# Kernel optimization log

Hardware: AMD Instinct MI355X
Metric: run time of the kernel (lower is better)

## Reference

```python
import jax, jax.numpy as jnp
import numpy as np

B, N_Q, N_K, DIM = 4, 4096, 4096, 256
INNER = 64
N_TOPK = 3
MINUS_INF = -1e9


def setup_inputs() -> dict:
    key = jax.random.key(0)
    ks = jax.random.split(key, 5)
    q = jax.random.normal(ks[0], (B, N_Q, DIM), dtype=jnp.float32)
    k = jax.random.normal(ks[1], (B, N_K, DIM), dtype=jnp.float32)
    v = jax.random.normal(ks[2], (B, N_K, DIM), dtype=jnp.float32)
    Wq = jax.random.normal(ks[3], (DIM, INNER), dtype=jnp.float32) * 0.02
    Wk = jax.random.normal(ks[4], (DIM, INNER), dtype=jnp.float32) * 0.02
    return {"q": q, "k": k, "v": v, "Wq": Wq, "Wk": Wk}


def reference(q, k, v, Wq, Wk):
    # v is accepted but unused, matching the torch module.
    scale = INNER ** (-0.5)  # dim_head == inner_dim == 64
    qh = (q @ Wq) * scale            # [B, N_Q, 64]
    kh = k @ Wk                      # [B, N_K, 64]
    # heads = 1 -> scores [B, 1, N_Q, N_K]
    scores = jnp.einsum('bqd,bkd->bqk', qh, kh)[:, None]
    # torch.kthvalue(k=N_K - 3) == 4th-largest value per row
    thresh = jax.lax.top_k(scores, N_TOPK + 1)[0][..., N_TOPK:N_TOPK + 1]
    masked = jnp.where(scores < thresh, MINUS_INF, scores)
    return jax.nn.softmax(masked, axis=-1)
```

## Files before the change

kernel.cpp:

```cpp
#include <hip/hip_runtime.h>
#include <hip/hip_bf16.h>
#include <math.h>

typedef float v4f __attribute__((ext_vector_type(4)));
typedef short bf16x8 __attribute__((ext_vector_type(8)));
typedef float f32x16 __attribute__((ext_vector_type(16)));

#define BATCH 4
#define NQ 4096
#define NK 4096
#define DIM 256
#define INNER 64
#define NEG_INF (-3.0e38f)
#define CAP 64

__global__ __launch_bounds__(256) void proj_kernel(
    const float* __restrict__ q, const float* __restrict__ k,
    const float* __restrict__ Wq, const float* __restrict__ Wk,
    float* __restrict__ qh, float* __restrict__ kh,
    ushort* __restrict__ qhb, ushort* __restrict__ khb)
{
  __shared__ float xs[32 * 260];
  const int bid = blockIdx.x;
  const bool isq = bid < 512;
  const float* X   = isq ? q : k;
  const float* W   = isq ? Wq : Wk;
  float*   out     = isq ? qh : kh;
  const float scale = isq ? 0.125f : 1.0f;
  const int row0 = (isq ? bid : bid - 512) * 32;
  const int t = threadIdx.x;

  #pragma unroll
  for (int it = 0; it < 8; ++it) {
    int idx = it * 256 + t;
    int r = idx >> 6, dq = idx & 63;
    v4f v = *reinterpret_cast<const v4f*>(X + (size_t)(row0 + r) * DIM + dq * 4);
    *reinterpret_cast<v4f*>(&xs[r * 260 + dq * 4]) = v;
  }
  __syncthreads();

  const int i0 = (t & 15) * 4;
  const int rg = t >> 4;
  float acc[2][4];
  #pragma unroll
  for (int p = 0; p < 2; ++p)
    #pragma unroll
    for (int i = 0; i < 4; ++i) acc[p][i] = 0.f;

  for (int d0 = 0; d0 < DIM; d0 += 4) {
    v4f w0 = *reinterpret_cast<const v4f*>(W + (d0 + 0) * INNER + i0);
    v4f w1 = *reinterpret_cast<const v4f*>(W + (d0 + 1) * INNER + i0);
    v4f w2 = *reinterpret_cast<const v4f*>(W + (d0 + 2) * INNER + i0);
    v4f w3 = *reinterpret_cast<const v4f*>(W + (d0 + 3) * INNER + i0);
    #pragma unroll
    for (int p = 0; p < 2; ++p) {
      v4f x = *reinterpret_cast<const v4f*>(&xs[(rg + 16 * p) * 260 + d0]);
      #pragma unroll
      for (int i = 0; i < 4; ++i) {
        float bs = x[0] * w0[i];
        bs = fmaf(x[1], w1[i], bs);
        bs = fmaf(x[2], w2[i], bs);
        bs = fmaf(x[3], w3[i], bs);
        acc[p][i] += bs;
      }
    }
  }

  const int d  = i0 >> 4;
  const int hi = (i0 >> 3) & 1;
  const int e0 = i0 & 7;
  #pragma unroll
  for (int p = 0; p < 2; ++p) {
    v4f o;
    ushort ob[4];
    #pragma unroll
    for (int i = 0; i < 4; ++i) {
      o[i] = acc[p][i] * scale;
      __hip_bfloat16 h = __float2bfloat16(o[i]);
      ob[i] = *reinterpret_cast<ushort*>(&h);
    }
    int rr = rg + 16 * p;
    size_t row = (size_t)(row0 + rr);
    *reinterpret_cast<v4f*>(out + row * INNER + i0) = o;
    if (isq) {
      *reinterpret_cast<uint2*>(qhb + row * INNER + i0) =
          *reinterpret_cast<uint2*>(ob);
    } else {
      size_t off = (size_t)(bid - 512) * 2048 + d * 512 + hi * 256 + rr * 8 + e0;
      *reinterpret_cast<uint2*>(khb + off) = *reinterpret_cast<uint2*>(ob);
    }
  }
}

__device__ __forceinline__ void insert5(float (&v)[5], int (&ix)[5], float x, int xi) {
  bool g0 = x > v[0], g1 = x > v[1], g2 = x > v[2], g3 = x > v[3];
  v[4]  = g3 ? v[3] : x;                 ix[4] = g3 ? ix[3] : xi;
  v[3]  = g3 ? (g2 ? v[2] : x) : v[3];   ix[3] = g3 ? (g2 ? ix[2] : xi) : ix[3];
  v[2]  = g2 ? (g1 ? v[1] : x) : v[2];   ix[2] = g2 ? (g1 ? ix[1] : xi) : ix[2];
  v[1]  = g1 ? (g0 ? v[0] : x) : v[1];   ix[1] = g1 ? (g0 ? ix[0] : xi) : ix[1];
  v[0]  = g0 ? x : v[0];                 ix[0] = g0 ? xi : ix[0];
}

__device__ __forceinline__ void insert8v(float (&v)[8], float x) {
  bool g0 = x > v[0], g1 = x > v[1], g2 = x > v[2], g3 = x > v[3];
  bool g4 = x > v[4], g5 = x > v[5], g6 = x > v[6];
  v[7] = g6 ? v[6] : x;
  v[6] = g6 ? (g5 ? v[5] : x) : v[6];
  v[5] = g5 ? (g4 ? v[4] : x) : v[5];
  v[4] = g4 ? (g3 ? v[3] : x) : v[4];
  v[3] = g3 ? (g2 ? v[2] : x) : v[3];
  v[2] = g2 ? (g1 ? v[1] : x) : v[2];
  v[1] = g1 ? (g0 ? v[0] : x) : v[1];
  v[0] = g0 ? x : v[0];
}

__global__ __launch_bounds__(512) void filter_kernel(
    const ushort* __restrict__ qhb, const ushort* __restrict__ khb,
    const float* __restrict__ qh, const float* __restrict__ kh,
    float* __restrict__ out)
{
  __shared__ float qhf[32][68];
  __shared__ float sm[32][16];
  __shared__ float tau[32];
  __shared__ int   cnt[32];
  __shared__ int   cand[32][CAP];
  __shared__ float exactv[32][CAP];
  __shared__ float w5[32][5];
  __shared__ int   id5[32][6];

  const int t   = threadIdx.x;
  const int bid = blockIdx.x;
  const int wg  = (bid & 7) * 64 + (bid >> 3);
  const int b   = wg >> 7;
  const int q0  = (wg & 127) * 32;
  const int qg  = t >> 6;
  const int kg  = t & 63;
  const int ln  = kg & 31;
  const int hi  = kg >> 5;

  float* obase = out + ((size_t)b * NQ + q0) * (size_t)NK;
  const v4f z = {0.f, 0.f, 0.f, 0.f};

  if (t < 256) {
    int row = t >> 3, c8 = (t & 7) * 8;
    const float* src = qh + ((size_t)b * NQ + q0 + row) * INNER + c8;
    *reinterpret_cast<v4f*>(&qhf[row][c8])     = *reinterpret_cast<const v4f*>(src);
    *reinterpret_cast<v4f*>(&qhf[row][c8 + 4]) = *reinterpret_cast<const v4f*>(src + 4);
  }
  if (t < 32) cnt[t] = 0;

  const ushort* qptr = qhb + ((size_t)b * NQ + q0 + ln) * INNER + hi * 8;
  bf16x8 qf0 = *reinterpret_cast<const bf16x8*>(qptr);
  bf16x8 qf1 = *reinterpret_cast<const bf16x8*>(qptr + 16);
  bf16x8 qf2 = *reinterpret_cast<const bf16x8*>(qptr + 32);
  bf16x8 qf3 = *reinterpret_cast<const bf16x8*>(qptr + 48);

  const ushort* ktile = khb + ((size_t)b * 128 + qg * 16) * 2048;

  float smax = NEG_INF;
  for (int t16 = 0; t16 < 16; ++t16) {
    const ushort* tb = ktile + (size_t)t16 * 2048;
    bf16x8 k0 = *reinterpret_cast<const bf16x8*>(tb +        kg * 8);
    bf16x8 k1 = *reinterpret_cast<const bf16x8*>(tb +  512 + kg * 8);
    bf16x8 k2 = *reinterpret_cast<const bf16x8*>(tb + 1024 + kg * 8);
    bf16x8 k3 = *reinterpret_cast<const bf16x8*>(tb + 1536 + kg * 8);

    *reinterpret_cast<v4f*>(obase + (size_t)(t16 * 2)     * 2048 + t * 4) = z;
    *reinterpret_cast<v4f*>(obase + (size_t)(t16 * 2 + 1) * 2048 + t * 4) = z;

    f32x16 acc = {0.f, 0.f, 0.f, 0.f, 0.f, 0.f, 0.f, 0.f,
                  0.f, 0.f, 0.f, 0.f, 0.f, 0.f, 0.f, 0.f};
    acc = __builtin_amdgcn_mfma_f32_32x32x16_bf16(k0, qf0, acc, 0, 0, 0);
    acc = __builtin_amdgcn_mfma_f32_32x32x16_bf16(k1, qf1, acc, 0, 0, 0);
    acc = __builtin_amdgcn_mfma_f32_32x32x16_bf16(k2, qf2, acc, 0, 0, 0);
    acc = __builtin_amdgcn_mfma_f32_32x32x16_bf16(k3, qf3, acc, 0, 0, 0);

    float m0 = fmaxf(fmaxf(acc[0],  acc[1]),  fmaxf(acc[2],  acc[3]));
    float m1 = fmaxf(fmaxf(acc[4],  acc[5]),  fmaxf(acc[6],  acc[7]));
    float m2 = fmaxf(fmaxf(acc[8],  acc[9]),  fmaxf(acc[10], acc[11]));
    float m3 = fmaxf(fmaxf(acc[12], acc[13]), fmaxf(acc[14], acc[15]));
    smax = fmaxf(smax, fmaxf(fmaxf(m0, m1), fmaxf(m2, m3)));
  }
  sm[ln][qg * 2 + hi] = smax;
  __syncthreads();

  if (t < 32) {
    float rv[8];
    #pragma unroll
    for (int j = 0; j < 8; ++j) rv[j] = NEG_INF;
    #pragma unroll
    for (int s = 0; s < 16; ++s) {
      float x = sm[t][s];
      if (x > rv[7]) insert8v(rv, x);
    }
    tau[t] = rv[7];
  }
  __syncthreads();

  const float tl = tau[ln];
  for (int t16 = 0; t16 < 16; ++t16) {
    const ushort* tb = ktile + (size_t)t16 * 2048;
    bf16x8 k0 = *reinterpret_cast<const bf16x8*>(tb +        kg * 8);
    bf16x8 k1 = *reinterpret_cast<const bf16x8*>(tb +  512 + kg * 8);
    bf16x8 k2 = *reinterpret_cast<const bf16x8*>(tb + 1024 + kg * 8);
    bf16x8 k3 = *reinterpret_cast<const bf16x8*>(tb + 1536 + kg * 8);

    *reinterpret_cast<v4f*>(obase + (size_t)(32 + t16 * 2)     * 2048 + t * 4) = z;
    *reinterpret_cast<v4f*>(obase + (size_t)(32 + t16 * 2 + 1) * 2048 + t * 4) = z;

    f32x16 acc = {0.f, 0.f, 0.f, 0.f, 0.f, 0.f, 0.f, 0.f,
                  0.f, 0.f, 0.f, 0.f, 0.f, 0.f, 0.f, 0.f};
    acc = __builtin_amdgcn_mfma_f32_32x32x16_bf16(k0, qf0, acc, 0, 0, 0);
    acc = __builtin_amdgcn_mfma_f32_32x32x16_bf16(k1, qf1, acc, 0, 0, 0);
    acc = __builtin_amdgcn_mfma_f32_32x32x16_bf16(k2, qf2, acc, 0, 0, 0);
    acc = __builtin_amdgcn_mfma_f32_32x32x16_bf16(k3, qf3, acc, 0, 0, 0);

    const int kb0 = qg * 512 + t16 * 32 + 4 * hi;
#define CHK(r) { float x_ = acc[r]; \
                 if (x_ >= tl) { \
                   int p_ = atomicAdd(&cnt[ln], 1); \
                   if (p_ < CAP) cand[ln][p_] = kb0 + ((r) & 3) + 8 * ((r) >> 2); } }
    CHK(0)  CHK(1)  CHK(2)  CHK(3)
    CHK(4)  CHK(5)  CHK(6)  CHK(7)
    CHK(8)  CHK(9)  CHK(10) CHK(11)
    CHK(12) CHK(13) CHK(14) CHK(15)
#undef CHK
  }
  __syncthreads();

  {
    int row = t >> 4, j0 = t & 15;
    int n = min(cnt[row], CAP);
    for (int jj = j0; jj < n; jj += 16) {
      int idx = cand[row][jj];
      const float* kcol = kh + ((size_t)b * NK + idx) * INNER;
      float acc = 0.f;
      #pragma unroll
      for (int dd = 0; dd < INNER; dd += 4) {
        v4f kv = *reinterpret_cast<const v4f*>(kcol + dd);
        v4f qv = *reinterpret_cast<const v4f*>(&qhf[row][dd]);
        float bs = qv[0] * kv[0];
        bs = fmaf(qv[1], kv[1], bs);
        bs = fmaf(qv[2], kv[2], bs);
        bs = fmaf(qv[3], kv[3], bs);
        acc += bs;
      }
      exactv[row][jj] = acc;
    }
  }
  __syncthreads();

  if (t < 32) {
    int n = min(cnt[t], CAP);
    float rv[5]; int ri[5];
    #pragma unroll
    for (int j = 0; j < 5; ++j) { rv[j] = NEG_INF; ri[j] = 0; }
    for (int j = 0; j < n; ++j) {
      float x = exactv[t][j];
      if (x > rv[4]) insert5(rv, ri, x, cand[t][j]);
    }
    bool inc4 = (rv[4] >= rv[3]);
    float e1 = expf(rv[1] - rv[0]);
    float e2 = expf(rv[2] - rv[0]);
    float e3 = expf(rv[3] - rv[0]);
    float e4 = inc4 ? expf(rv[4] - rv[0]) : 0.0f;
    float inv = 1.0f / (1.0f + e1 + e2 + e3 + e4);
    w5[t][0] = inv;      w5[t][1] = e1 * inv;  w5[t][2] = e2 * inv;
    w5[t][3] = e3 * inv; w5[t][4] = e4 * inv;
    #pragma unroll
    for (int j = 0; j < 5; ++j) id5[t][j] = ri[j];
    id5[t][5] = inc4 ? 5 : 4;
  }
  __syncthreads();

  if (t < 160) {
    int row = t / 5, j = t % 5;
    if (j < id5[row][5])
      obase[(size_t)row * NK + id5[row][j]] = w5[row][j];
  }
}

extern "C" void kernel_launch(void* const* d_in, const int* in_sizes, int n_in,
                              void* d_out, int out_size, void* d_ws, size_t ws_size,
                              hipStream_t stream) {
  const float* q  = (const float*)d_in[0];
  const float* k  = (const float*)d_in[1];
  const float* Wq = (const float*)d_in[3];
  const float* Wk = (const float*)d_in[4];

  const size_t NE = (size_t)BATCH * NQ * INNER;
  float*  qh  = (float*)d_ws;
  float*  kh  = qh + NE;
  ushort* qhb = (ushort*)(kh + NE);
  ushort* khb = qhb + NE;

  proj_kernel<<<1024, 256, 0, stream>>>(q, k, Wq, Wk, qh, kh, qhb, khb);
  filter_kernel<<<512, 512, 0, stream>>>(qhb, khb, qh, kh, (float*)d_out);
}
```

Baseline: 120.5 us.

## Specialize extra warps to zero the output with nontemporal stores

The filter kernel grows from 512 to 768 threads. The original 512 threads now only compute scores, thresholds and the top-k softmax. The extra 256 threads zero the block's 32 output rows with nontemporal vector stores, split into five phases that match the compute path's five barriers, so every zero lands before the final scatter of softmax weights. The aim is to overlap the large zero-fill write traffic with the MFMA and selection work and to keep those stores out of cache. The larger launch bound lowers the per-thread register budget, which could cause spills or reduce occupancy.

```diff
diff --git a/kernel.cpp b/kernel.cpp
--- a/kernel.cpp
+++ b/kernel.cpp
@@ -114,7 +114,7 @@
   v[0] = g0 ? x : v[0];
 }
 
-__global__ __launch_bounds__(512) void filter_kernel(
+__global__ __launch_bounds__(768) void filter_kernel(
     const ushort* __restrict__ qhb, const ushort* __restrict__ khb,
     const float* __restrict__ qh, const float* __restrict__ kh,
     float* __restrict__ out)
@@ -133,150 +133,171 @@
   const int wg  = (bid & 7) * 64 + (bid >> 3);
   const int b   = wg >> 7;
   const int q0  = (wg & 127) * 32;
-  const int qg  = t >> 6;
-  const int kg  = t & 63;
-  const int ln  = kg & 31;
-  const int hi  = kg >> 5;
 
   float* obase = out + ((size_t)b * NQ + q0) * (size_t)NK;
   const v4f z = {0.f, 0.f, 0.f, 0.f};
 
-  if (t < 256) {
-    int row = t >> 3, c8 = (t & 7) * 8;
-    const float* src = qh + ((size_t)b * NQ + q0 + row) * INNER + c8;
-    *reinterpret_cast<v4f*>(&qhf[row][c8])     = *reinterpret_cast<const v4f*>(src);
-    *reinterpret_cast<v4f*>(&qhf[row][c8 + 4]) = *reinterpret_cast<const v4f*>(src + 4);
-  }
-  if (t < 32) cnt[t] = 0;
-
-  const ushort* qptr = qhb + ((size_t)b * NQ + q0 + ln) * INNER + hi * 8;
-  bf16x8 qf0 = *reinterpret_cast<const bf16x8*>(qptr);
-  bf16x8 qf1 = *reinterpret_cast<const bf16x8*>(qptr + 16);
-  bf16x8 qf2 = *reinterpret_cast<const bf16x8*>(qptr + 32);
-  bf16x8 qf3 = *reinterpret_cast<const bf16x8*>(qptr + 48);
-
-  const ushort* ktile = khb + ((size_t)b * 128 + qg * 16) * 2048;
-
-  float smax = NEG_INF;
-  for (int t16 = 0; t16 < 16; ++t16) {
-    const ushort* tb = ktile + (size_t)t16 * 2048;
-    bf16x8 k0 = *reinterpret_cast<const bf16x8*>(tb +        kg * 8);
-    bf16x8 k1 = *reinterpret_cast<const bf16x8*>(tb +  512 + kg * 8);
-    bf16x8 k2 = *reinterpret_cast<const bf16x8*>(tb + 1024 + kg * 8);
-    bf16x8 k3 = *reinterpret_cast<const bf16x8*>(tb + 1536 + kg * 8);
-
-    *reinterpret_cast<v4f*>(obase + (size_t)(t16 * 2)     * 2048 + t * 4) = z;
-    *reinterpret_cast<v4f*>(obase + (size_t)(t16 * 2 + 1) * 2048 + t * 4) = z;
-
-    f32x16 acc = {0.f, 0.f, 0.f, 0.f, 0.f, 0.f, 0.f, 0.f,
-                  0.f, 0.f, 0.f, 0.f, 0.f, 0.f, 0.f, 0.f};
-    acc = __builtin_amdgcn_mfma_f32_32x32x16_bf16(k0, qf0, acc, 0, 0, 0);
-    acc = __builtin_amdgcn_mfma_f32_32x32x16_bf16(k1, qf1, acc, 0, 0, 0);
-    acc = __builtin_amdgcn_mfma_f32_32x32x16_bf16(k2, qf2, acc, 0, 0, 0);
-    acc = __builtin_amdgcn_mfma_f32_32x32x16_bf16(k3, qf3, acc, 0, 0, 0);
-
-    float m0 = fmaxf(fmaxf(acc[0],  acc[1]),  fmaxf(acc[2],  acc[3]));
-    float m1 = fmaxf(fmaxf(acc[4],  acc[5]),  fmaxf(acc[6],  acc[7]));
-    float m2 = fmaxf(fmaxf(acc[8],  acc[9]),  fmaxf(acc[10], acc[11]));
-    float m3 = fmaxf(fmaxf(acc[12], acc[13]), fmaxf(acc[14], acc[15]));
-    smax = fmaxf(smax, fmaxf(fmaxf(m0, m1), fmaxf(m2, m3)));
-  }
-  sm[ln][qg * 2 + hi] = smax;
-  __syncthreads();
-
-  if (t < 32) {
-    float rv[8];
-    #pragma unroll
-    for (int j = 0; j < 8; ++j) rv[j] = NEG_INF;
-    #pragma unroll
-    for (int s = 0; s < 16; ++s) {
-      float x = sm[t][s];
-      if (x > rv[7]) insert8v(rv, x);
-    }
-    tau[t] = rv[7];
-  }
-  __syncthreads();
-
-  const float tl = tau[ln];
-  for (int t16 = 0; t16 < 16; ++t16) {
-    const ushort* tb = ktile + (size_t)t16 * 2048;
-    bf16x8 k0 = *reinterpret_cast<const bf16x8*>(tb +        kg * 8);
-    bf16x8 k1 = *reinterpret_cast<const bf16x8*>(tb +  512 + kg * 8);
-    bf16x8 k2 = *reinterpret_cast<const bf16x8*>(tb + 1024 + kg * 8);
-    bf16x8 k3 = *reinterpret_cast<const bf16x8*>(tb + 1536 + kg * 8);
-
-    *reinterpret_cast<v4f*>(obase + (size_t)(32 + t16 * 2)     * 2048 + t * 4) = z;
-    *reinterpret_cast<v4f*>(obase + (size_t)(32 + t16 * 2 + 1) * 2048 + t * 4) = z;
-
-    f32x16 acc = {0.f, 0.f, 0.f, 0.f, 0.f, 0.f, 0.f, 0.f,
-                  0.f, 0.f, 0.f, 0.f, 0.f, 0.f, 0.f, 0.f};
-    acc = __builtin_amdgcn_mfma_f32_32x32x16_bf16(k0, qf0, acc, 0, 0, 0);
-    acc = __builtin_amdgcn_mfma_f32_32x32x16_bf16(k1, qf1, acc, 0, 0, 0);
-    acc = __builtin_amdgcn_mfma_f32_32x32x16_bf16(k2, qf2, acc, 0, 0, 0);
-    acc = __builtin_amdgcn_mfma_f32_32x32x16_bf16(k3, qf3, acc, 0, 0, 0);
-
-    const int kb0 = qg * 512 + t16 * 32 + 4 * hi;
+  if (t < 512) {
+    const int qg  = t >> 6;
+    const int kg  = t & 63;
+    const int ln  = kg & 31;
+    const int hi  = kg >> 5;
+
+    if (t < 256) {
+      int row = t >> 3, c8 = (t & 7) * 8;
+      const float* src = qh + ((size_t)b * NQ + q0 + row) * INNER + c8;
+      *reinterpret_cast<v4f*>(&qhf[row][c8])     = *reinterpret_cast<const v4f*>(src);
+      *reinterpret_cast<v4f*>(&qhf[row][c8 + 4]) = *reinterpret_cast<const v4f*>(src + 4);
+    }
+    if (t < 32) cnt[t] = 0;
+
+    const ushort* qptr = qhb + ((size_t)b * NQ + q0 + ln) * INNER + hi * 8;
+    bf16x8 qf0 = *reinterpret_cast<const bf16x8*>(qptr);
+    bf16x8 qf1 = *reinterpret_cast<const bf16x8*>(qptr + 16);
+    bf16x8 qf2 = *reinterpret_cast<const bf16x8*>(qptr + 32);
+    bf16x8 qf3 = *reinterpret_cast<const bf16x8*>(qptr + 48);
+
+    const ushort* ktile = khb + ((size_t)b * 128 + qg * 16) * 2048;
+
+    float smax = NEG_INF;
+    for (int t16 = 0; t16 < 16; ++t16) {
+      const ushort* tb = ktile + (size_t)t16 * 2048;
+      bf16x8 k0 = *reinterpret_cast<const bf16x8*>(tb +        kg * 8);
+      bf16x8 k1 = *reinterpret_cast<const bf16x8*>(tb +  512 + kg * 8);
+      bf16x8 k2 = *reinterpret_cast<const bf16x8*>(tb + 1024 + kg * 8);
+      bf16x8 k3 = *reinterpret_cast<const bf16x8*>(tb + 1536 + kg * 8);
+
+      f32x16 acc = {0.f, 0.f, 0.f, 0.f, 0.f, 0.f, 0.f, 0.f,
+                    0.f, 0.f, 0.f, 0.f, 0.f, 0.f, 0.f, 0.f};
+      acc = __builtin_amdgcn_mfma_f32_32x32x16_bf16(k0, qf0, acc, 0, 0, 0);
+      acc = __builtin_amdgcn_mfma_f32_32x32x16_bf16(k1, qf1, acc, 0, 0, 0);
+      acc = __builtin_amdgcn_mfma_f32_32x32x16_bf16(k2, qf2, acc, 0, 0, 0);
+      acc = __builtin_amdgcn_mfma_f32_32x32x16_bf16(k3, qf3, acc, 0, 0, 0);
+
+      float m0 = fmaxf(fmaxf(acc[0],  acc[1]),  fmaxf(acc[2],  acc[3]));
+      float m1 = fmaxf(fmaxf(acc[4],  acc[5]),  fmaxf(acc[6],  acc[7]));
+      float m2 = fmaxf(fmaxf(acc[8],  acc[9]),  fmaxf(acc[10], acc[11]));
+      float m3 = fmaxf(fmaxf(acc[12], acc[13]), fmaxf(acc[14], acc[15]));
+      smax = fmaxf(smax, fmaxf(fmaxf(m0, m1), fmaxf(m2, m3)));
+    }
+    sm[ln][qg * 2 + hi] = smax;
+    __syncthreads();
+
+    if (t < 32) {
+      float rv[8];
+      #pragma unroll
+      for (int j = 0; j < 8; ++j) rv[j] = NEG_INF;
+      #pragma unroll
+      for (int s = 0; s < 16; ++s) {
+        float x = sm[t][s];
+        if (x > rv[7]) insert8v(rv, x);
+      }
+      tau[t] = rv[7];
+    }
+    __syncthreads();
+
+    const float tl = tau[ln];
+    for (int t16 = 0; t16 < 16; ++t16) {
+      const ushort* tb = ktile + (size_t)t16 * 2048;
+      bf16x8 k0 = *reinterpret_cast<const bf16x8*>(tb +        kg * 8);
+      bf16x8 k1 = *reinterpret_cast<const bf16x8*>(tb +  512 + kg * 8);
+      bf16x8 k2 = *reinterpret_cast<const bf16x8*>(tb + 1024 + kg * 8);
+      bf16x8 k3 = *reinterpret_cast<const bf16x8*>(tb + 1536 + kg * 8);
+
+      f32x16 acc = {0.f, 0.f, 0.f, 0.f, 0.f, 0.f, 0.f, 0.f,
+                    0.f, 0.f, 0.f, 0.f, 0.f, 0.f, 0.f, 0.f};
+      acc = __builtin_amdgcn_mfma_f32_32x32x16_bf16(k0, qf0, acc, 0, 0, 0);
+      acc = __builtin_amdgcn_mfma_f32_32x32x16_bf16(k1, qf1, acc, 0, 0, 0);
+      acc = __builtin_amdgcn_mfma_f32_32x32x16_bf16(k2, qf2, acc, 0, 0, 0);
+      acc = __builtin_amdgcn_mfma_f32_32x32x16_bf16(k3, qf3, acc, 0, 0, 0);
+
+      const int kb0 = qg * 512 + t16 * 32 + 4 * hi;
 #define CHK(r) { float x_ = acc[r]; \
                  if (x_ >= tl) { \
                    int p_ = atomicAdd(&cnt[ln], 1); \
                    if (p_ < CAP) cand[ln][p_] = kb0 + ((r) & 3) + 8 * ((r) >> 2); } }
-    CHK(0)  CHK(1)  CHK(2)  CHK(3)
-    CHK(4)  CHK(5)  CHK(6)  CHK(7)
-    CHK(8)  CHK(9)  CHK(10) CHK(11)
-    CHK(12) CHK(13) CHK(14) CHK(15)
+      CHK(0)  CHK(1)  CHK(2)  CHK(3)
+      CHK(4)  CHK(5)  CHK(6)  CHK(7)
+      CHK(8)  CHK(9)  CHK(10) CHK(11)
+      CHK(12) CHK(13) CHK(14) CHK(15)
 #undef CHK
-  }
-  __syncthreads();
-
-  {
-    int row = t >> 4, j0 = t & 15;
-    int n = min(cnt[row], CAP);
-    for (int jj = j0; jj < n; jj += 16) {
-      int idx = cand[row][jj];
-      const float* kcol = kh + ((size_t)b * NK + idx) * INNER;
-      float acc = 0.f;
-      #pragma unroll
-      for (int dd = 0; dd < INNER; dd += 4) {
-        v4f kv = *reinterpret_cast<const v4f*>(kcol + dd);
-        v4f qv = *reinterpret_cast<const v4f*>(&qhf[row][dd]);
-        float bs = qv[0] * kv[0];
-        bs = fmaf(qv[1], kv[1], bs);
-        bs = fmaf(qv[2], kv[2], bs);
-        bs = fmaf(qv[3], kv[3], bs);
-        acc += bs;
+    }
+    __syncthreads();
+
+    {
+      int row = t >> 4, j0 = t & 15;
+      int n = min(cnt[row], CAP);
+      for (int jj = j0; jj < n; jj += 16) {
+        int idx = cand[row][jj];
+        const float* kcol = kh + ((size_t)b * NK + idx) * INNER;
+        float acc = 0.f;
+        #pragma unroll
+        for (int dd = 0; dd < INNER; dd += 4) {
+          v4f kv = *reinterpret_cast<const v4f*>(kcol + dd);
+          v4f qv = *reinterpret_cast<const v4f*>(&qhf[row][dd]);
+          float bs = qv[0] * kv[0];
+          bs = fmaf(qv[1], kv[1], bs);
+          bs = fmaf(qv[2], kv[2], bs);
+          bs = fmaf(qv[3], kv[3], bs);
+          acc += bs;
+        }
+        exactv[row][jj] = acc;
       }
-      exactv[row][jj] = acc;
-    }
-  }
-  __syncthreads();
-
-  if (t < 32) {
-    int n = min(cnt[t], CAP);
-    float rv[5]; int ri[5];
-    #pragma unroll
-    for (int j = 0; j < 5; ++j) { rv[j] = NEG_INF; ri[j] = 0; }
-    for (int j = 0; j < n; ++j) {
-      float x = exactv[t][j];
-      if (x > rv[4]) insert5(rv, ri, x, cand[t][j]);
-    }
-    bool inc4 = (rv[4] >= rv[3]);
-    float e1 = expf(rv[1] - rv[0]);
-    float e2 = expf(rv[2] - rv[0]);
-    float e3 = expf(rv[3] - rv[0]);
-    float e4 = inc4 ? expf(rv[4] - rv[0]) : 0.0f;
-    float inv = 1.0f / (1.0f + e1 + e2 + e3 + e4);
-    w5[t][0] = inv;      w5[t][1] = e1 * inv;  w5[t][2] = e2 * inv;
-    w5[t][3] = e3 * inv; w5[t][4] = e4 * inv;
-    #pragma unroll
-    for (int j = 0; j < 5; ++j) id5[t][j] = ri[j];
-    id5[t][5] = inc4 ? 5 : 4;
-  }
-  __syncthreads();
-
-  if (t < 160) {
-    int row = t / 5, j = t % 5;
-    if (j < id5[row][5])
-      obase[(size_t)row * NK + id5[row][j]] = w5[row][j];
+    }
+    __syncthreads();
+
+    if (t < 32) {
+      int n = min(cnt[t], CAP);
+      float rv[5]; int ri[5];
+      #pragma unroll
+      for (int j = 0; j < 5; ++j) { rv[j] = NEG_INF; ri[j] = 0; }
+      for (int j = 0; j < n; ++j) {
+        float x = exactv[t][j];
+        if (x > rv[4]) insert5(rv, ri, x, cand[t][j]);
+      }
+      bool inc4 = (rv[4] >= rv[3]);
+      float e1 = expf(rv[1] - rv[0]);
+      float e2 = expf(rv[2] - rv[0]);
+      float e3 = expf(rv[3] - rv[0]);
+      float e4 = inc4 ? expf(rv[4] - rv[0]) : 0.0f;
+      float inv = 1.0f / (1.0f + e1 + e2 + e3 + e4);
+      w5[t][0] = inv;      w5[t][1] = e1 * inv;  w5[t][2] = e2 * inv;
+      w5[t][3] = e3 * inv; w5[t][4] = e4 * inv;
+      #pragma unroll
+      for (int j = 0; j < 5; ++j) id5[t][j] = ri[j];
+      id5[t][5] = inc4 ? 5 : 4;
+    }
+    __syncthreads();
+
+    if (t < 160) {
+      int row = t / 5, j = t % 5;
+      if (j < id5[row][5])
+        obase[(size_t)row * NK + id5[row][j]] = w5[row][j];
+    }
+  } else {
+    const int tz = t - 512;
+    v4f* zp = reinterpret_cast<v4f*>(obase);
+    int it = 0;
+    #pragma unroll 2
+    for (int u = 0; u < 26; ++u, ++it)
+      __builtin_nontemporal_store(z, zp + it * 256 + tz);
+    __syncthreads();
+    #pragma unroll 2
+    for (int u = 0; u < 26; ++u, ++it)
+      __builtin_nontemporal_store(z, zp + it * 256 + tz);
+    __syncthreads();
+    #pragma unroll 2
+    for (int u = 0; u < 26; ++u, ++it)
+      __builtin_nontemporal_store(z, zp + it * 256 + tz);
+    __syncthreads();
+    #pragma unroll 2
+    for (int u = 0; u < 25; ++u, ++it)
+      __builtin_nontemporal_store(z, zp + it * 256 + tz);
+    __syncthreads();
+    #pragma unroll 2
+    for (int u = 0; u < 25; ++u, ++it)
+      __builtin_nontemporal_store(z, zp + it * 256 + tz);
+    __syncthreads();
   }
 }
 
@@ -295,5 +316,5 @@
   ushort* khb = qhb + NE;
 
   proj_kernel<<<1024, 256, 0, stream>>>(q, k, Wq, Wk, qh, kh, qhb, khb);
-  filter_kernel<<<512, 512, 0, stream>>>(qhb, khb, qh, kh, (float*)d_out);
-}
+  filter_kernel<<<512, 768, 0, stream>>>(qhb, khb, qh, kh, (float*)d_out);
+}
```

New measurement: 142.8 us. 1.19x slower.
